# Performance work log

Measured on AMD Instinct MI355X. Metric: run time of the kernel, lower is better.

Reference implementation:

```python
import jax, jax.numpy as jnp
import numpy as np

B, C, H, W = 2, 512, 64, 64
NUM_HEADS = 8
HEAD_DIM = C // NUM_HEADS


def setup_inputs() -> dict:
    key = jax.random.key(0)
    ks = jax.random.split(key, 6)
    s = 1.0 / np.sqrt(C)
    return {
        "x": jax.random.normal(ks[0], (B, C, H, W), dtype=jnp.float32),
        "w_qkv": jax.random.normal(ks[1], (3 * C, C), dtype=jnp.float32) * s,
        "b_qkv": jax.random.normal(ks[2], (3 * C,), dtype=jnp.float32) * 0.01,
        "w_out": jax.random.normal(ks[3], (C, C), dtype=jnp.float32) * s,
        "b_out": jax.random.normal(ks[4], (C,), dtype=jnp.float32) * 0.01,
        "gamma": jax.random.normal(ks[5], (1,), dtype=jnp.float32) * 0.1,
    }


def reference(x, w_qkv, b_qkv, w_out, b_out, gamma):
    b, c, h, w = x.shape
    n = h * w
    nh, hd = NUM_HEADS, HEAD_DIM
    # 1x1 conv QKV projection == per-pixel linear
    qkv = jnp.einsum('oc,bchw->bohw', w_qkv, x) + b_qkv[None, :, None, None]
    qkv = qkv.reshape(b, 3, nh, hd, n)  # [B,3,nh,hd,N]
    q = qkv[:, 0].transpose(0, 1, 3, 2)  # [B,nh,N,hd]
    k = qkv[:, 1]                        # [B,nh,hd,N]
    v = qkv[:, 2].transpose(0, 1, 3, 2)  # [B,nh,N,hd]
    scale = hd ** -0.5
    attn = jnp.einsum('bhnd,bhdm->bhnm', q, k) * scale  # [B,nh,N,N]
    attn = jax.nn.softmax(attn, axis=-1)
    out = jnp.einsum('bhnm,bhmd->bhnd', attn, v)  # [B,nh,N,hd]
    out = out.transpose(0, 1, 3, 2).reshape(b, c, h, w)  # [B,C,H,W]
    out = jnp.einsum('oc,bchw->bohw', w_out, out) + b_out[None, :, None, None]
    return gamma[0] * out + x
```

## Files before the change

### kernel.cpp

```cpp
#include <hip/hip_runtime.h>
#include <hip/hip_bf16.h>

typedef __bf16 bf16_t;
typedef __bf16 bf16x8 __attribute__((ext_vector_type(8)));
typedef __bf16 bf16x4 __attribute__((ext_vector_type(4)));
typedef float floatx4 __attribute__((ext_vector_type(4)));
typedef float f32x16 __attribute__((ext_vector_type(16)));

#define MFMA_BF16(a, b, c) __builtin_amdgcn_mfma_f32_16x16x32_bf16((a), (b), (c), 0, 0, 0)
#define MFMA32(a, b, c) __builtin_amdgcn_mfma_f32_32x32x16_bf16((a), (b), (c), 0, 0, 0)

static constexpr int CB = 512;
static constexpr int NB = 4096;

__device__ __forceinline__ unsigned cvtpk_bf16(float lo, float hi_) {
  unsigned r;
  asm("v_cvt_pk_bf16_f32 %0, %1, %2" : "=v"(r) : "v"(lo), "v"(hi_));
  return r;
}
__device__ __forceinline__ void plswap(unsigned& x, unsigned& y) {
  asm volatile("v_permlane32_swap_b32 %0, %1" : "+v"(x), "+v"(y));
}
__device__ __forceinline__ float exp2_fast(float x) {
  float r;
  asm("v_exp_f32 %0, %1" : "=v"(r) : "v"(x));
  return r;
}

#define GLOAD_LDS16(gsrc, ldst)                                              \
  __builtin_amdgcn_global_load_lds(                                          \
      (const __attribute__((address_space(1))) void*)(gsrc),                 \
      (__attribute__((address_space(3))) void*)(ldst), 16, 0, 0)

__global__ __launch_bounds__(256) void k_transpose(const float* __restrict__ x,
                                                   bf16_t* __restrict__ xT) {
  __shared__ __align__(16) bf16_t T[64 * 72];
  const int t = threadIdx.x;
  const int b = blockIdx.z, c0 = blockIdx.y * 64, n0 = blockIdx.x * 64;
  {
    const int cl = t >> 4, nl = (t & 15) * 4;
#pragma unroll
    for (int p = 0; p < 4; ++p) {
      const int c = cl + p * 16;
      const float4 v = *reinterpret_cast<const float4*>(
          x + ((size_t)(b * CB + c0 + c) * NB) + n0 + nl);
      T[(nl + 0) * 72 + c] = (bf16_t)v.x;
      T[(nl + 1) * 72 + c] = (bf16_t)v.y;
      T[(nl + 2) * 72 + c] = (bf16_t)v.z;
      T[(nl + 3) * 72 + c] = (bf16_t)v.w;
    }
  }
  __syncthreads();
  {
    const int nr = t >> 2, ch = t & 3;
    bf16_t* op = xT + ((size_t)(b * NB + n0 + nr) * CB) + c0;
#pragma unroll
    for (int p = 0; p < 2; ++p) {
      bf16x8 v = *reinterpret_cast<const bf16x8*>(&T[nr * 72 + ch * 8 + p * 32]);
      *reinterpret_cast<bf16x8*>(op + ch * 8 + p * 32) = v;
    }
  }
}

__global__ __launch_bounds__(256) void k_qkv(const float* __restrict__ W,
                                             const float* __restrict__ bias,
                                             const bf16_t* __restrict__ xT,
                                             bf16_t* __restrict__ Qb,
                                             bf16_t* __restrict__ Kb,
                                             bf16_t* __restrict__ Vb) {
  __shared__ __align__(16) bf16_t As[128 * 40];
  __shared__ __align__(16) bf16_t Bs[128 * 40];
  const int t = threadIdx.x;
  const int lane = t & 63, wv = t >> 6;
  const int g = lane >> 4, c = lane & 15;
  const int wm = wv >> 1, wn = wv & 1;
  const int o0 = blockIdx.x * 128, n0 = blockIdx.y * 128;
  const int b = blockIdx.z;

  floatx4 acc[4][4] = {};

  const float* Ap = W + (size_t)o0 * CB;
  const bf16_t* Bp = xT + ((size_t)b * NB + n0) * CB;

  for (int kt = 0; kt < CB; kt += 32) {
    {
      const int row = t >> 3, c4 = (t & 7) * 4;
#pragma unroll
      for (int p = 0; p < 4; ++p) {
        const int r = row + p * 32;
        const float4 v = *reinterpret_cast<const float4*>(Ap + (size_t)r * CB + kt + c4);
        bf16x4 w4;
        w4[0] = (bf16_t)v.x; w4[1] = (bf16_t)v.y; w4[2] = (bf16_t)v.z; w4[3] = (bf16_t)v.w;
        *reinterpret_cast<bf16x4*>(&As[r * 40 + c4]) = w4;
      }
    }
    {
      const int row = t >> 2, ch = t & 3;
#pragma unroll
      for (int p = 0; p < 2; ++p) {
        const int r = row + p * 64;
        bf16x8 v = *reinterpret_cast<const bf16x8*>(Bp + (size_t)r * CB + kt + ch * 8);
        *reinterpret_cast<bf16x8*>(&Bs[r * 40 + ch * 8]) = v;
      }
    }
    __syncthreads();
    bf16x8 af[4], bfr[4];
#pragma unroll
    for (int i = 0; i < 4; ++i)
      af[i] = *reinterpret_cast<const bf16x8*>(&As[(wm * 64 + i * 16 + c) * 40 + g * 8]);
#pragma unroll
    for (int j = 0; j < 4; ++j)
      bfr[j] = *reinterpret_cast<const bf16x8*>(&Bs[(wn * 64 + j * 16 + c) * 40 + g * 8]);
#pragma unroll
    for (int i = 0; i < 4; ++i)
#pragma unroll
      for (int j = 0; j < 4; ++j)
        acc[i][j] = MFMA_BF16(af[i], bfr[j], acc[i][j]);
    __syncthreads();
  }

  const int which = o0 >> 9;
#pragma unroll
  for (int i = 0; i < 4; ++i) {
    const int ob = o0 + wm * 64 + i * 16 + 4 * g;
    float bias4[4];
#pragma unroll
    for (int r = 0; r < 4; ++r) bias4[r] = bias[ob + r];
    const int h = (ob >> 6) & 7;
    const int d0 = ob & 63;
#pragma unroll
    for (int j = 0; j < 4; ++j) {
      const int n = n0 + wn * 64 + j * 16 + c;
      if (which == 2) {
        bf16_t* vp = Vb + (size_t)(b * 8 + h) * 64 * NB + n;
#pragma unroll
        for (int r = 0; r < 4; ++r)
          vp[(size_t)(d0 + r) * NB] = (bf16_t)(acc[i][j][r] + bias4[r]);
      } else {
        bf16_t* qp = (which == 0 ? Qb : Kb) + ((size_t)(b * 8 + h) * NB + n) * 64 + d0;
        bf16x4 pk;
#pragma unroll
        for (int r = 0; r < 4; ++r) pk[r] = (bf16_t)(acc[i][j][r] + bias4[r]);
        *reinterpret_cast<bf16x4*>(qp) = pk;
      }
    }
  }
}

__global__ __launch_bounds__(256, 3) void k_attn(const bf16_t* __restrict__ Qb,
                                                 const bf16_t* __restrict__ Kb,
                                                 const bf16_t* __restrict__ Vb,
                                                 bf16_t* __restrict__ P0,
                                                 bf16_t* __restrict__ P1,
                                                 float* __restrict__ lsum) {
  __shared__ __align__(16) bf16_t Kl[3][4096];
  __shared__ __align__(16) bf16_t Vl[3][4096];
  const int t = threadIdx.x, lane = t & 63, w = t >> 6;
  const int q31 = lane & 31, hi = lane >> 5;

  const int bid = blockIdx.x;
  const int xcd = bid & 7, j = bid >> 3;
  const int bh = xcd * 2 + (j >> 6);
  const int rest = j & 63;
  const int qt = rest >> 1, half = rest & 1;
  const int q0 = qt * 128 + w * 32;
  const int kvbase = half * 2048;

  const size_t base = (size_t)bh * NB * 64;
  const bf16_t* Qp = Qb + base;
  const bf16_t* Kp = Kb + base;
  const bf16_t* Vp = Vb + base;
  bf16_t* Op = (half ? P1 : P0) + base;

  const float SC = 0.125f * 1.44269504088896340736f;
  const float FM = 8.0f;

  bf16x8 qf[4];
#pragma unroll
  for (int ks = 0; ks < 4; ++ks) {
    bf16x8 q = *reinterpret_cast<const bf16x8*>(Qp + (size_t)(q0 + q31) * 64 + ks * 16 + hi * 8);
#pragma unroll
    for (int e = 0; e < 8; ++e) q[e] = (bf16_t)((float)q[e] * SC);
    qf[ks] = q;
  }

  bf16x8 ones;
#pragma unroll
  for (int e = 0; e < 8; ++e) ones[e] = (bf16_t)1.0f;

  const int srow0 = t >> 3, srow1 = srow0 + 32;
  const int sc0 = ((t & 7) ^ (srow0 & 7)) * 8;
  const int sc1 = ((t & 7) ^ (srow1 & 7)) * 8;
  const bf16_t* ksrc0 = Kp + (size_t)(kvbase + srow0) * 64 + sc0;
  const bf16_t* ksrc1 = Kp + (size_t)(kvbase + srow1) * 64 + sc1;
  const bf16_t* vsrc0 = Vp + (size_t)srow0 * NB + kvbase + sc0;
  const bf16_t* vsrc1 = Vp + (size_t)srow1 * NB + kvbase + sc1;

#define STAGE_TILE(ss, slot)                                                  \
  do {                                                                        \
    const size_t ko_ = (size_t)(ss) * 64 * 64;                                \
    const int vo_ = (ss) * 64;                                                \
    bf16_t* kd_ = &Kl[(slot)][0];                                             \
    bf16_t* vd_ = &Vl[(slot)][0];                                             \
    GLOAD_LDS16(ksrc0 + ko_, kd_ + w * 512);                                  \
    GLOAD_LDS16(ksrc1 + ko_, kd_ + 2048 + w * 512);                           \
    GLOAD_LDS16(vsrc0 + vo_, vd_ + w * 512);                                  \
    GLOAD_LDS16(vsrc1 + vo_, vd_ + 2048 + w * 512);                           \
  } while (0)

  int c16r[4];
#pragma unroll
  for (int ks = 0; ks < 4; ++ks) c16r[ks] = ((ks * 2 + hi) ^ (q31 & 7)) * 8;

  f32x16 O0 = {}, O1 = {}, lacc = {};
  f32x16 NEGM;
#pragma unroll
  for (int r = 0; r < 16; ++r) NEGM[r] = -FM;

  STAGE_TILE(0, 0);
  STAGE_TILE(1, 1);
  asm volatile("s_waitcnt vmcnt(4)" ::: "memory");
  __builtin_amdgcn_s_barrier();
  __builtin_amdgcn_sched_barrier(0);

  int cur = 0;
  for (int s = 0; s < 32; ++s) {
    const bf16_t* Kbuf = &Kl[cur][0];
    const bf16_t* Vbuf = &Vl[cur][0];
    if (s < 30) {
      int nx2 = cur + 2; if (nx2 >= 3) nx2 -= 3;
      STAGE_TILE(s + 2, nx2);
    }
    f32x16 st0 = NEGM, st1 = NEGM;
    __builtin_amdgcn_s_setprio(1);
#pragma unroll
    for (int ks = 0; ks < 4; ++ks) {
      bf16x8 kf0 = *reinterpret_cast<const bf16x8*>(&Kbuf[q31 * 64 + c16r[ks]]);
      bf16x8 kf1 = *reinterpret_cast<const bf16x8*>(&Kbuf[(32 + q31) * 64 + c16r[ks]]);
      st0 = MFMA32(kf0, qf[ks], st0);
      st1 = MFMA32(kf1, qf[ks], st1);
    }
    __builtin_amdgcn_s_setprio(0);

#pragma unroll
    for (int r = 0; r < 16; ++r) st0[r] = exp2_fast(st0[r]);
#pragma unroll
    for (int r = 0; r < 16; ++r) st1[r] = exp2_fast(st1[r]);

    __builtin_amdgcn_s_setprio(1);
#pragma unroll
    for (int ks = 0; ks < 4; ++ks) {
      const f32x16& P = (ks < 2) ? st0 : st1;
      const int rb = (ks & 1) * 8;
      unsigned x0 = cvtpk_bf16(P[rb + 0], P[rb + 1]);
      unsigned y0 = cvtpk_bf16(P[rb + 4], P[rb + 5]);
      unsigned x1 = cvtpk_bf16(P[rb + 2], P[rb + 3]);
      unsigned y1 = cvtpk_bf16(P[rb + 6], P[rb + 7]);
      plswap(x0, y0);
      plswap(x1, y1);
      union { unsigned u[4]; bf16x8 v; } pa;
      pa.u[0] = x0; pa.u[1] = x1; pa.u[2] = y0; pa.u[3] = y1;
      bf16x8 vf0 = *reinterpret_cast<const bf16x8*>(&Vbuf[q31 * 64 + c16r[ks]]);
      bf16x8 vf1 = *reinterpret_cast<const bf16x8*>(&Vbuf[(32 + q31) * 64 + c16r[ks]]);
      O0 = MFMA32(pa.v, vf0, O0);
      O1 = MFMA32(pa.v, vf1, O1);
      lacc = MFMA32(pa.v, ones, lacc);
    }
    __builtin_amdgcn_s_setprio(0);

    if (s < 31) {
      if (s < 30)
        asm volatile("s_waitcnt vmcnt(4) lgkmcnt(0)" ::: "memory");
      else
        asm volatile("s_waitcnt vmcnt(0) lgkmcnt(0)" ::: "memory");
      __builtin_amdgcn_s_barrier();
      __builtin_amdgcn_sched_barrier(0);
    }
    ++cur; if (cur >= 3) cur = 0;
  }
#undef STAGE_TILE

#pragma unroll
  for (int r = 0; r < 16; ++r) {
    const int n = q0 + (r & 3) + 8 * (r >> 2) + 4 * hi;
    bf16_t* op = Op + ((size_t)n) * 64 + q31;
    op[0]  = (bf16_t)O0[r];
    op[32] = (bf16_t)O1[r];
  }
  if (q31 == 0) {
    float* lp = lsum + (size_t)(half * 16 + bh) * NB;
#pragma unroll
    for (int r = 0; r < 16; ++r) {
      const int row = (r & 3) + 8 * (r >> 2) + 4 * hi;
      lp[q0 + row] = lacc[r];
    }
  }
}

__global__ __launch_bounds__(256) void k_out(const float* __restrict__ W,
                                             const float* __restrict__ bias,
                                             const bf16_t* __restrict__ P0,
                                             const bf16_t* __restrict__ P1,
                                             const float* __restrict__ lsum,
                                             const float* __restrict__ x,
                                             const float* __restrict__ gamma,
                                             float* __restrict__ y) {
  __shared__ __align__(16) bf16_t As[128 * 40];
  __shared__ __align__(16) bf16_t Bs[128 * 40];
  const int t = threadIdx.x;
  const int lane = t & 63, wv = t >> 6;
  const int g = lane >> 4, c = lane & 15;
  const int wm = wv >> 1, wn = wv & 1;
  const int o0 = blockIdx.x * 128, n0 = blockIdx.y * 128;
  const int b = blockIdx.z;

  floatx4 acc[4][4] = {};

  const float* Ap = W + (size_t)o0 * CB;

  for (int kt = 0; kt < CB; kt += 32) {
    {
      const int row = t >> 3, c4 = (t & 7) * 4;
#pragma unroll
      for (int p = 0; p < 4; ++p) {
        const int r = row + p * 32;
        const float4 v = *reinterpret_cast<const float4*>(Ap + (size_t)r * CB + kt + c4);
        bf16x4 w4;
        w4[0] = (bf16_t)v.x; w4[1] = (bf16_t)v.y; w4[2] = (bf16_t)v.z; w4[3] = (bf16_t)v.w;
        *reinterpret_cast<bf16x4*>(&As[r * 40 + c4]) = w4;
      }
    }
    {
      const int row = t >> 2, ch = t & 3;
      const int cc = kt + ch * 8;
      const int h = cc >> 6, d = cc & 63;
#pragma unroll
      for (int p = 0; p < 2; ++p) {
        const int r = row + p * 64;
        const int n = n0 + r;
        const size_t li = (size_t)(b * 8 + h) * NB + n;
        const size_t idx = li * 64 + d;
        const bf16x8 oa = *reinterpret_cast<const bf16x8*>(P0 + idx);
        const bf16x8 ob = *reinterpret_cast<const bf16x8*>(P1 + idx);
        const float rl = 1.0f / (lsum[li] + lsum[li + 16 * NB]);
        bf16x8 o;
#pragma unroll
        for (int e = 0; e < 8; ++e)
          o[e] = (bf16_t)(((float)oa[e] + (float)ob[e]) * rl);
        *reinterpret_cast<bf16x8*>(&Bs[r * 40 + ch * 8]) = o;
      }
    }
    __syncthreads();
    bf16x8 af[4], bfr[4];
#pragma unroll
    for (int i = 0; i < 4; ++i)
      af[i] = *reinterpret_cast<const bf16x8*>(&As[(wm * 64 + i * 16 + c) * 40 + g * 8]);
#pragma unroll
    for (int j = 0; j < 4; ++j)
      bfr[j] = *reinterpret_cast<const bf16x8*>(&Bs[(wn * 64 + j * 16 + c) * 40 + g * 8]);
#pragma unroll
    for (int i = 0; i < 4; ++i)
#pragma unroll
      for (int j = 0; j < 4; ++j)
        acc[i][j] = MFMA_BF16(af[i], bfr[j], acc[i][j]);
    __syncthreads();
  }

  const float gm = gamma[0];
#pragma unroll
  for (int i = 0; i < 4; ++i) {
    const int ob = o0 + wm * 64 + i * 16 + 4 * g;
    float bias4[4];
#pragma unroll
    for (int r = 0; r < 4; ++r) bias4[r] = bias[ob + r];
#pragma unroll
    for (int j = 0; j < 4; ++j) {
      const int n = n0 + wn * 64 + j * 16 + c;
      const float* xp = x + ((size_t)(b * CB + ob) * NB) + n;
      float* yp = y + ((size_t)(b * CB + ob) * NB) + n;
#pragma unroll
      for (int r = 0; r < 4; ++r)
        yp[(size_t)r * NB] = gm * (acc[i][j][r] + bias4[r]) + xp[(size_t)r * NB];
    }
  }
}

extern "C" void kernel_launch(void* const* d_in, const int* in_sizes, int n_in,
                              void* d_out, int out_size, void* d_ws, size_t ws_size,
                              hipStream_t stream) {
  const float* x      = (const float*)d_in[0];
  const float* w_qkv  = (const float*)d_in[1];
  const float* b_qkv  = (const float*)d_in[2];
  const float* w_out  = (const float*)d_in[3];
  const float* b_out  = (const float*)d_in[4];
  const float* gamma  = (const float*)d_in[5];
  float* y = (float*)d_out;

  const size_t CH = 4194304;
  bf16_t* Wp = (bf16_t*)d_ws;
  bf16_t* Qb = Wp;
  bf16_t* Kb = Wp + CH;
  bf16_t* Vb = Wp + 2 * CH;
  bf16_t* P0 = Wp + 3 * CH;
  bf16_t* xT = Wp + 4 * CH;
  bf16_t* P1 = Wp + 4 * CH;
  float*  lsum = (float*)(Wp + 5 * CH);

  k_transpose<<<dim3(64, 8, 2), 256, 0, stream>>>(x, xT);
  k_qkv<<<dim3(12, 32, 2), 256, 0, stream>>>(w_qkv, b_qkv, xT, Qb, Kb, Vb);
  k_attn<<<dim3(1024), 256, 0, stream>>>(Qb, Kb, Vb, P0, P1, lsum);
  k_out<<<dim3(4, 32, 2), 256, 0, stream>>>(w_out, b_out, P0, P1, lsum, x, gamma, y);
}
```

Measured before the change: 153.9 us.

## Fuse input transpose into QKV GEMM and double-buffer 128-key attention tiles

Removes the separate transpose kernel: the QKV GEMM now reads fp32 x directly, packs pairs of channels into bf16 and writes the transposed tile into shared memory itself. This drops one launch and a full intermediate write and read of xT. The attention kernel moves from a 3-slot ring of 64-key tiles to a 2-slot double buffer of 128-key tiles, which halves the barrier count. In exchange, each stage waits with vmcnt(0), leaving less prefetch slack, and the occupancy hint falls from 3 to 2 blocks because shared memory use grows.

After: 155.9 us. No clear change (+1.3%).

```diff
diff --git a/kernel.cpp b/kernel.cpp
--- a/kernel.cpp
+++ b/kernel.cpp
@@ -32,39 +32,9 @@
       (const __attribute__((address_space(1))) void*)(gsrc),                 \
       (__attribute__((address_space(3))) void*)(ldst), 16, 0, 0)
 
-__global__ __launch_bounds__(256) void k_transpose(const float* __restrict__ x,
-                                                   bf16_t* __restrict__ xT) {
-  __shared__ __align__(16) bf16_t T[64 * 72];
-  const int t = threadIdx.x;
-  const int b = blockIdx.z, c0 = blockIdx.y * 64, n0 = blockIdx.x * 64;
-  {
-    const int cl = t >> 4, nl = (t & 15) * 4;
-#pragma unroll
-    for (int p = 0; p < 4; ++p) {
-      const int c = cl + p * 16;
-      const float4 v = *reinterpret_cast<const float4*>(
-          x + ((size_t)(b * CB + c0 + c) * NB) + n0 + nl);
-      T[(nl + 0) * 72 + c] = (bf16_t)v.x;
-      T[(nl + 1) * 72 + c] = (bf16_t)v.y;
-      T[(nl + 2) * 72 + c] = (bf16_t)v.z;
-      T[(nl + 3) * 72 + c] = (bf16_t)v.w;
-    }
-  }
-  __syncthreads();
-  {
-    const int nr = t >> 2, ch = t & 3;
-    bf16_t* op = xT + ((size_t)(b * NB + n0 + nr) * CB) + c0;
-#pragma unroll
-    for (int p = 0; p < 2; ++p) {
-      bf16x8 v = *reinterpret_cast<const bf16x8*>(&T[nr * 72 + ch * 8 + p * 32]);
-      *reinterpret_cast<bf16x8*>(op + ch * 8 + p * 32) = v;
-    }
-  }
-}
-
 __global__ __launch_bounds__(256) void k_qkv(const float* __restrict__ W,
                                              const float* __restrict__ bias,
-                                             const bf16_t* __restrict__ xT,
+                                             const float* __restrict__ x,
                                              bf16_t* __restrict__ Qb,
                                              bf16_t* __restrict__ Kb,
                                              bf16_t* __restrict__ Vb) {
@@ -80,7 +50,7 @@
   floatx4 acc[4][4] = {};
 
   const float* Ap = W + (size_t)o0 * CB;
-  const bf16_t* Bp = xT + ((size_t)b * NB + n0) * CB;
+  const float* xb = x + (size_t)b * CB * NB + n0;
 
   for (int kt = 0; kt < CB; kt += 32) {
     {
@@ -95,12 +65,23 @@
       }
     }
     {
-      const int row = t >> 2, ch = t & 3;
-#pragma unroll
-      for (int p = 0; p < 2; ++p) {
-        const int r = row + p * 64;
-        bf16x8 v = *reinterpret_cast<const bf16x8*>(Bp + (size_t)r * CB + kt + ch * 8);
-        *reinterpret_cast<bf16x8*>(&Bs[r * 40 + ch * 8]) = v;
+      const int p2 = (t & 15) * 2;
+      const int nq0 = t >> 4;
+      const float* xr0 = xb + (size_t)(kt + p2) * NB;
+      const float* xr1 = xr0 + NB;
+#pragma unroll
+      for (int it = 0; it < 2; ++it) {
+        const int nn = (nq0 + 16 * it) * 4;
+        const float4 a = *reinterpret_cast<const float4*>(xr0 + nn);
+        const float4 bv = *reinterpret_cast<const float4*>(xr1 + nn);
+        const unsigned u0 = cvtpk_bf16(a.x, bv.x);
+        const unsigned u1 = cvtpk_bf16(a.y, bv.y);
+        const unsigned u2 = cvtpk_bf16(a.z, bv.z);
+        const unsigned u3 = cvtpk_bf16(a.w, bv.w);
+        *reinterpret_cast<unsigned*>(&Bs[(nn + 0) * 40 + p2]) = u0;
+        *reinterpret_cast<unsigned*>(&Bs[(nn + 1) * 40 + p2]) = u1;
+        *reinterpret_cast<unsigned*>(&Bs[(nn + 2) * 40 + p2]) = u2;
+        *reinterpret_cast<unsigned*>(&Bs[(nn + 3) * 40 + p2]) = u3;
       }
     }
     __syncthreads();
@@ -147,14 +128,14 @@
   }
 }
 
-__global__ __launch_bounds__(256, 3) void k_attn(const bf16_t* __restrict__ Qb,
+__global__ __launch_bounds__(256, 2) void k_attn(const bf16_t* __restrict__ Qb,
                                                  const bf16_t* __restrict__ Kb,
                                                  const bf16_t* __restrict__ Vb,
                                                  bf16_t* __restrict__ P0,
                                                  bf16_t* __restrict__ P1,
                                                  float* __restrict__ lsum) {
-  __shared__ __align__(16) bf16_t Kl[3][4096];
-  __shared__ __align__(16) bf16_t Vl[3][4096];
+  __shared__ __align__(16) bf16_t Kl[2][2][4096];
+  __shared__ __align__(16) bf16_t Vl[2][2][4096];
   const int t = threadIdx.x, lane = t & 63, w = t >> 6;
   const int q31 = lane & 31, hi = lane >> 5;
 
@@ -196,16 +177,22 @@
   const bf16_t* vsrc0 = Vp + (size_t)srow0 * NB + kvbase + sc0;
   const bf16_t* vsrc1 = Vp + (size_t)srow1 * NB + kvbase + sc1;
 
-#define STAGE_TILE(ss, slot)                                                  \
+#define STAGE128(ss, bufi)                                                    \
   do {                                                                        \
-    const size_t ko_ = (size_t)(ss) * 64 * 64;                                \
-    const int vo_ = (ss) * 64;                                                \
-    bf16_t* kd_ = &Kl[(slot)][0];                                             \
-    bf16_t* vd_ = &Vl[(slot)][0];                                             \
-    GLOAD_LDS16(ksrc0 + ko_, kd_ + w * 512);                                  \
-    GLOAD_LDS16(ksrc1 + ko_, kd_ + 2048 + w * 512);                           \
-    GLOAD_LDS16(vsrc0 + vo_, vd_ + w * 512);                                  \
-    GLOAD_LDS16(vsrc1 + vo_, vd_ + 2048 + w * 512);                           \
+    const size_t ko_ = (size_t)(ss) * 8192;                                   \
+    const int vo_ = (ss) * 128;                                               \
+    bf16_t* kd0_ = &Kl[(bufi)][0][0];                                         \
+    bf16_t* kd1_ = &Kl[(bufi)][1][0];                                         \
+    bf16_t* vd0_ = &Vl[(bufi)][0][0];                                         \
+    bf16_t* vd1_ = &Vl[(bufi)][1][0];                                         \
+    GLOAD_LDS16(ksrc0 + ko_, kd0_ + w * 512);                                 \
+    GLOAD_LDS16(ksrc1 + ko_, kd0_ + 2048 + w * 512);                          \
+    GLOAD_LDS16(ksrc0 + ko_ + 4096, kd1_ + w * 512);                          \
+    GLOAD_LDS16(ksrc1 + ko_ + 4096, kd1_ + 2048 + w * 512);                   \
+    GLOAD_LDS16(vsrc0 + vo_, vd0_ + w * 512);                                 \
+    GLOAD_LDS16(vsrc1 + vo_, vd0_ + 2048 + w * 512);                         \
+    GLOAD_LDS16(vsrc0 + vo_ + 64, vd1_ + w * 512);                            \
+    GLOAD_LDS16(vsrc1 + vo_ + 64, vd1_ + 2048 + w * 512);                     \
   } while (0)
 
   int c16r[4];
@@ -217,68 +204,63 @@
 #pragma unroll
   for (int r = 0; r < 16; ++r) NEGM[r] = -FM;
 
-  STAGE_TILE(0, 0);
-  STAGE_TILE(1, 1);
-  asm volatile("s_waitcnt vmcnt(4)" ::: "memory");
+  STAGE128(0, 0);
+  asm volatile("s_waitcnt vmcnt(0)" ::: "memory");
   __builtin_amdgcn_s_barrier();
   __builtin_amdgcn_sched_barrier(0);
 
-  int cur = 0;
-  for (int s = 0; s < 32; ++s) {
-    const bf16_t* Kbuf = &Kl[cur][0];
-    const bf16_t* Vbuf = &Vl[cur][0];
-    if (s < 30) {
-      int nx2 = cur + 2; if (nx2 >= 3) nx2 -= 3;
-      STAGE_TILE(s + 2, nx2);
-    }
-    f32x16 st0 = NEGM, st1 = NEGM;
-    __builtin_amdgcn_s_setprio(1);
-#pragma unroll
-    for (int ks = 0; ks < 4; ++ks) {
-      bf16x8 kf0 = *reinterpret_cast<const bf16x8*>(&Kbuf[q31 * 64 + c16r[ks]]);
-      bf16x8 kf1 = *reinterpret_cast<const bf16x8*>(&Kbuf[(32 + q31) * 64 + c16r[ks]]);
-      st0 = MFMA32(kf0, qf[ks], st0);
-      st1 = MFMA32(kf1, qf[ks], st1);
-    }
-    __builtin_amdgcn_s_setprio(0);
-
-#pragma unroll
-    for (int r = 0; r < 16; ++r) st0[r] = exp2_fast(st0[r]);
-#pragma unroll
-    for (int r = 0; r < 16; ++r) st1[r] = exp2_fast(st1[r]);
-
-    __builtin_amdgcn_s_setprio(1);
-#pragma unroll
-    for (int ks = 0; ks < 4; ++ks) {
-      const f32x16& P = (ks < 2) ? st0 : st1;
-      const int rb = (ks & 1) * 8;
-      unsigned x0 = cvtpk_bf16(P[rb + 0], P[rb + 1]);
-      unsigned y0 = cvtpk_bf16(P[rb + 4], P[rb + 5]);
-      unsigned x1 = cvtpk_bf16(P[rb + 2], P[rb + 3]);
-      unsigned y1 = cvtpk_bf16(P[rb + 6], P[rb + 7]);
-      plswap(x0, y0);
-      plswap(x1, y1);
-      union { unsigned u[4]; bf16x8 v; } pa;
-      pa.u[0] = x0; pa.u[1] = x1; pa.u[2] = y0; pa.u[3] = y1;
-      bf16x8 vf0 = *reinterpret_cast<const bf16x8*>(&Vbuf[q31 * 64 + c16r[ks]]);
-      bf16x8 vf1 = *reinterpret_cast<const bf16x8*>(&Vbuf[(32 + q31) * 64 + c16r[ks]]);
-      O0 = MFMA32(pa.v, vf0, O0);
-      O1 = MFMA32(pa.v, vf1, O1);
-      lacc = MFMA32(pa.v, ones, lacc);
-    }
-    __builtin_amdgcn_s_setprio(0);
-
-    if (s < 31) {
-      if (s < 30)
-        asm volatile("s_waitcnt vmcnt(4) lgkmcnt(0)" ::: "memory");
-      else
-        asm volatile("s_waitcnt vmcnt(0) lgkmcnt(0)" ::: "memory");
+  int buf = 0;
+  for (int s = 0; s < 16; ++s) {
+    if (s < 15) STAGE128(s + 1, buf ^ 1);
+#pragma unroll
+    for (int sub = 0; sub < 2; ++sub) {
+      const bf16_t* Kbuf = &Kl[buf][sub][0];
+      const bf16_t* Vbuf = &Vl[buf][sub][0];
+      f32x16 st0 = NEGM, st1 = NEGM;
+      __builtin_amdgcn_s_setprio(1);
+#pragma unroll
+      for (int ks = 0; ks < 4; ++ks) {
+        bf16x8 kf0 = *reinterpret_cast<const bf16x8*>(&Kbuf[q31 * 64 + c16r[ks]]);
+        bf16x8 kf1 = *reinterpret_cast<const bf16x8*>(&Kbuf[(32 + q31) * 64 + c16r[ks]]);
+        st0 = MFMA32(kf0, qf[ks], st0);
+        st1 = MFMA32(kf1, qf[ks], st1);
+      }
+      __builtin_amdgcn_s_setprio(0);
+
+#pragma unroll
+      for (int r = 0; r < 16; ++r) st0[r] = exp2_fast(st0[r]);
+#pragma unroll
+      for (int r = 0; r < 16; ++r) st1[r] = exp2_fast(st1[r]);
+
+      __builtin_amdgcn_s_setprio(1);
+#pragma unroll
+      for (int ks = 0; ks < 4; ++ks) {
+        const f32x16& P = (ks < 2) ? st0 : st1;
+        const int rb = (ks & 1) * 8;
+        unsigned x0 = cvtpk_bf16(P[rb + 0], P[rb + 1]);
+        unsigned y0 = cvtpk_bf16(P[rb + 4], P[rb + 5]);
+        unsigned x1 = cvtpk_bf16(P[rb + 2], P[rb + 3]);
+        unsigned y1 = cvtpk_bf16(P[rb + 6], P[rb + 7]);
+        plswap(x0, y0);
+        plswap(x1, y1);
+        union { unsigned u[4]; bf16x8 v; } pa;
+        pa.u[0] = x0; pa.u[1] = x1; pa.u[2] = y0; pa.u[3] = y1;
+        bf16x8 vf0 = *reinterpret_cast<const bf16x8*>(&Vbuf[q31 * 64 + c16r[ks]]);
+        bf16x8 vf1 = *reinterpret_cast<const bf16x8*>(&Vbuf[(32 + q31) * 64 + c16r[ks]]);
+        O0 = MFMA32(pa.v, vf0, O0);
+        O1 = MFMA32(pa.v, vf1, O1);
+        lacc = MFMA32(pa.v, ones, lacc);
+      }
+      __builtin_amdgcn_s_setprio(0);
+    }
+    if (s < 15) {
+      asm volatile("s_waitcnt vmcnt(0) lgkmcnt(0)" ::: "memory");
       __builtin_amdgcn_s_barrier();
       __builtin_amdgcn_sched_barrier(0);
     }
-    ++cur; if (cur >= 3) cur = 0;
-  }
-#undef STAGE_TILE
+    buf ^= 1;
+  }
+#undef STAGE128
 
 #pragma unroll
   for (int r = 0; r < 16; ++r) {
@@ -402,12 +384,10 @@
   bf16_t* Kb = Wp + CH;
   bf16_t* Vb = Wp + 2 * CH;
   bf16_t* P0 = Wp + 3 * CH;
-  bf16_t* xT = Wp + 4 * CH;
   bf16_t* P1 = Wp + 4 * CH;
   float*  lsum = (float*)(Wp + 5 * CH);
 
-  k_transpose<<<dim3(64, 8, 2), 256, 0, stream>>>(x, xT);
-  k_qkv<<<dim3(12, 32, 2), 256, 0, stream>>>(w_qkv, b_qkv, xT, Qb, Kb, Vb);
+  k_qkv<<<dim3(12, 32, 2), 256, 0, stream>>>(w_qkv, b_qkv, x, Qb, Kb, Vb);
   k_attn<<<dim3(1024), 256, 0, stream>>>(Qb, Kb, Vb, P0, P1, lsum);
   k_out<<<dim3(4, 32, 2), 256, 0, stream>>>(w_out, b_out, P0, P1, lsum, x, gamma, y);
 }
```
